# Kernel optimization log

Measured on AMD Instinct MI355X. Metric: run time of the kernel, lower is better.

Reference implementation:

```python
import jax, jax.numpy as jnp
import numpy as np

LN_EPS = 1e-5


def _segment_mean(vals, idx, num_segments):
    s = jax.ops.segment_sum(vals, idx, num_segments=num_segments)
    cnt = jax.ops.segment_sum(jnp.ones((vals.shape[0],), vals.dtype), idx, num_segments=num_segments)
    return s / jnp.maximum(cnt, 1.0)[:, None]


def _sage_layer(x, src, dst, W_l, b_l, W_r, gamma, beta):
    # PyG SAGEConv (mean aggr): out = lin_l(mean_{j in N(i)} x_j) + lin_r(x_i)
    N = x.shape[0]
    agg = _segment_mean(x[src], dst, N)                     # [N, in]
    h = agg @ W_l.T + b_l + x @ W_r.T                       # [N, out]
    mu = jnp.mean(h, axis=-1, keepdims=True)
    var = jnp.mean((h - mu) ** 2, axis=-1, keepdims=True)
    h = (h - mu) * jax.lax.rsqrt(var + LN_EPS) * gamma + beta
    return jax.nn.relu(h)                                   # dropout: eval mode (identity)


def setup_inputs() -> dict:
    key = jax.random.key(0)
    ks = jax.random.split(key, 20)
    N, E, IN, H, OUT, G, C = 50000, 600000, 128, 128, 64, 64, 2

    def glorot(k, fo, fi):
        lim = np.sqrt(6.0 / (fo + fi)).astype(np.float32)
        return jax.random.uniform(k, (fo, fi), jnp.float32, -lim, lim)

    inp = {
        'x': jax.random.normal(ks[0], (N, IN), jnp.float32),
        'edge_index': jax.random.randint(ks[1], (2, E), 0, N, jnp.int64),
        'batch': jnp.sort(jax.random.randint(ks[2], (N,), 0, G, jnp.int64)),
    }
    dims = [(IN, H), (H, H), (H, OUT)]
    for i, (fi, fo) in enumerate(dims):
        inp[f'Wl{i}'] = glorot(ks[3 + 4 * i], fo, fi)
        inp[f'bl{i}'] = jnp.zeros((fo,), jnp.float32)
        inp[f'Wr{i}'] = glorot(ks[4 + 4 * i], fo, fi)
        inp[f'g{i}'] = jnp.ones((fo,), jnp.float32)
        inp[f'be{i}'] = jnp.zeros((fo,), jnp.float32)
    inp['cW1'] = glorot(ks[16], H, 2 * OUT)
    inp['cb1'] = jnp.zeros((H,), jnp.float32)
    inp['cW2'] = glorot(ks[17], C, H)
    inp['cb2'] = jnp.zeros((C,), jnp.float32)
    return inp


def reference(x, edge_index, batch,
              Wl0, bl0, Wr0, g0, be0,
              Wl1, bl1, Wr1, g1, be1,
              Wl2, bl2, Wr2, g2, be2,
              cW1, cb1, cW2, cb2):
    src, dst = edge_index[0], edge_index[1]
    h = _sage_layer(x, src, dst, Wl0, bl0, Wr0, g0, be0)
    h = _sage_layer(h, src, dst, Wl1, bl1, Wr1, g1, be1)
    h = _sage_layer(h, src, dst, Wl2, bl2, Wr2, g2, be2)
    G = 64  # number of graphs
    x_mean = _segment_mean(h, batch, G)                     # [G, out]
    x_max = jax.ops.segment_max(h, batch, num_segments=G)   # [G, out]
    z = jnp.concatenate([x_mean, x_max], axis=-1)           # [G, 2*out]
    z = jax.nn.relu(z @ cW1.T + cb1)
    return z @ cW2.T + cb2                                  # [G, num_classes]
```

## Files before the change

kernel.cpp:

```cpp
#include <hip/hip_runtime.h>

typedef unsigned short ushort_t;
typedef short s16x8 __attribute__((ext_vector_type(8)));
typedef float f32x4 __attribute__((ext_vector_type(4)));

#define LN_EPS 1e-5f

__device__ __forceinline__ float b2f(ushort_t u) {
    return __uint_as_float(((unsigned)u) << 16);
}
__device__ __forceinline__ ushort_t f2b(float f) {
    unsigned b = __float_as_uint(f);
    b += 0x7FFFu + ((b >> 16) & 1u);
    return (ushort_t)(b >> 16);
}
__device__ __forceinline__ float ldf(const void* p, size_t i, int isF) {
    return isF ? ((const float*)p)[i] : b2f(((const ushort_t*)p)[i]);
}

__global__ void GraphSAGE_36026185678961_kernel() {}

__global__ void k_detect(const void* w0, const void* ei, int* __restrict__ flags) {
    int t = threadIdx.x;
    const ushort_t* u = (const ushort_t*)w0;
    int pass = 0;
    #pragma unroll
    for (int k = 0; k < 4; ++k) {
        ushort_t v = u[t * 4 + k];
        int ex = (v >> 7) & 0xFF;
        if (ex == 0 || (ex >= 0x60 && ex <= 0x7E)) pass++;
    }
    const unsigned* w = (const unsigned*)ei;
    int nz = (w[2 * t + 1] != 0u) ? 1 : 0;
    #pragma unroll
    for (int off = 32; off; off >>= 1) {
        pass += __shfl_down(pass, off, 64);
        nz += __shfl_down(nz, off, 64);
    }
    if (t == 0) {
        flags[0] = (pass < 205) ? 1 : 0;
        flags[1] = (nz == 0) ? 1 : 0;
    }
}

__global__ void k_zero(int* __restrict__ deg, float* __restrict__ Z, int N) {
    int i = blockIdx.x * blockDim.x + threadIdx.x;
    if (i < N) deg[i] = 0;
    if (i < 64 * 128) Z[i] = 0.f;
}

__global__ void k_xconv(const void* X, const int* __restrict__ flags,
                        ushort_t* __restrict__ XB, int total4) {
    int idx = blockIdx.x * blockDim.x + threadIdx.x;
    if (idx >= total4) return;
    if (flags[0]) {
        float4 v = ((const float4*)X)[idx];
        ushort4 o;
        o.x = f2b(v.x); o.y = f2b(v.y); o.z = f2b(v.z); o.w = f2b(v.w);
        ((ushort4*)XB)[idx] = o;
    } else {
        ((ushort4*)XB)[idx] = ((const ushort4*)X)[idx];
    }
}

__global__ void k_edges(const void* ei, int E, int N, const int* __restrict__ flags,
                        int* __restrict__ s32, int* __restrict__ d32, int* __restrict__ deg) {
    int e = blockIdx.x * blockDim.x + threadIdx.x;
    if (e >= E) return;
    int s, d;
    if (flags[1]) {
        const long long* p = (const long long*)ei;
        s = (int)p[e];
        d = (int)p[E + e];
    } else {
        const int* p = (const int*)ei;
        s = p[e];
        d = p[E + e];
    }
    s32[e] = s;
    d32[e] = d;
    if ((unsigned)d < (unsigned)N) atomicAdd(&deg[d], 1);
}

__global__ void k_scan1(const int* __restrict__ deg, int N,
                        int* __restrict__ rowptr, int* __restrict__ bsum) {
    __shared__ int wsum[4];
    __shared__ int wpre[4];
    int tid = threadIdx.x;
    int lane = tid & 63;
    int w = tid >> 6;
    int i = blockIdx.x * 256 + tid;
    int v = (i < N) ? deg[i] : 0;
    int x = v;
    #pragma unroll
    for (int off = 1; off < 64; off <<= 1) {
        int t = __shfl_up(x, off, 64);
        if (lane >= off) x += t;
    }
    if (lane == 63) wsum[w] = x;
    __syncthreads();
    if (tid == 0) {
        int a = wsum[0]; wpre[0] = a;
        a += wsum[1]; wpre[1] = a;
        a += wsum[2]; wpre[2] = a;
        a += wsum[3]; wpre[3] = a;
    }
    __syncthreads();
    int woff = (w == 0) ? 0 : wpre[w - 1];
    if (i < N) rowptr[i] = woff + x - v;
    if (tid == 0) bsum[blockIdx.x] = wpre[3];
}

__global__ void k_scan2(const int* __restrict__ bsum, int nb,
                        int* __restrict__ boff, int* __restrict__ rowptrN) {
    __shared__ int wsum[4];
    __shared__ int wpre[4];
    int tid = threadIdx.x;
    int lane = tid & 63;
    int w = tid >> 6;
    int run = 0;
    for (int base = 0; base < nb; base += 256) {
        int i = base + tid;
        int v = (i < nb) ? bsum[i] : 0;
        int x = v;
        #pragma unroll
        for (int off = 1; off < 64; off <<= 1) {
            int t = __shfl_up(x, off, 64);
            if (lane >= off) x += t;
        }
        if (lane == 63) wsum[w] = x;
        __syncthreads();
        if (tid == 0) {
            int a = wsum[0]; wpre[0] = a;
            a += wsum[1]; wpre[1] = a;
            a += wsum[2]; wpre[2] = a;
            a += wsum[3]; wpre[3] = a;
        }
        __syncthreads();
        int woff = (w == 0) ? 0 : wpre[w - 1];
        if (i < nb) boff[i] = run + woff + x - v;
        int tot = wpre[3];
        __syncthreads();
        run += tot;
    }
    if (tid == 0) *rowptrN = run;
}

__global__ void k_scan3(int* __restrict__ rowptr, const int* __restrict__ boff,
                        int* __restrict__ cursor, int N) {
    int i = blockIdx.x * 256 + threadIdx.x;
    if (i < N) {
        int r = rowptr[i] + boff[i >> 8];
        rowptr[i] = r;
        cursor[i] = r;
    }
}

__global__ void k_fill(const int* __restrict__ src, const int* __restrict__ dst, int E, int N,
                       int* __restrict__ cursor, int* __restrict__ col) {
    int e = blockIdx.x * blockDim.x + threadIdx.x;
    if (e < E) {
        int d = dst[e];
        if ((unsigned)d < (unsigned)N) {
            int p = atomicAdd(&cursor[d], 1);
            if ((unsigned)p < (unsigned)E) {
                int s = src[e];
                col[p] = ((unsigned)s < (unsigned)N) ? s : 0;
            }
        }
    }
}

__global__ void k_bounds(const void* batch, int N, int G, const int* __restrict__ flags,
                         int* __restrict__ bounds) {
    int g = threadIdx.x;
    if (g > G) return;
    int isL = flags[1];
    int lo = 0, hi = N;
    while (lo < hi) {
        int mid = (lo + hi) >> 1;
        int bv = isL ? (int)((const long long*)batch)[mid] : ((const int*)batch)[mid];
        if (bv < g) lo = mid + 1; else hi = mid;
    }
    bounds[g] = lo;
}

__global__ __launch_bounds__(256) void k_agg(
    const ushort_t* __restrict__ X, const int* __restrict__ rowptr,
    const int* __restrict__ col, ushort_t* __restrict__ AGG, int N) {
    int i = blockIdx.x * 4 + (threadIdx.x >> 6);
    if (i >= N) return;
    int l = threadIdx.x & 63;
    int half = l >> 5;
    int fq = l & 31;
    const ushort4* X4 = (const ushort4*)X;
    int s = rowptr[i], e = rowptr[i + 1];
    float a0 = 0.f, a1 = 0.f, a2 = 0.f, a3 = 0.f;
    int p = s + half;
    for (; p + 2 < e; p += 4) {
        int j0 = col[p], j1 = col[p + 2];
        ushort4 u0 = X4[(size_t)j0 * 32 + fq];
        ushort4 u1 = X4[(size_t)j1 * 32 + fq];
        a0 += b2f(u0.x) + b2f(u1.x);
        a1 += b2f(u0.y) + b2f(u1.y);
        a2 += b2f(u0.z) + b2f(u1.z);
        a3 += b2f(u0.w) + b2f(u1.w);
    }
    for (; p < e; p += 2) {
        int j = col[p];
        ushort4 u = X4[(size_t)j * 32 + fq];
        a0 += b2f(u.x); a1 += b2f(u.y); a2 += b2f(u.z); a3 += b2f(u.w);
    }
    a0 += __shfl_xor(a0, 32, 64);
    a1 += __shfl_xor(a1, 32, 64);
    a2 += __shfl_xor(a2, 32, 64);
    a3 += __shfl_xor(a3, 32, 64);
    if (half == 0) {
        int d = e - s;
        float inv = 1.f / (float)(d > 0 ? d : 1);
        ushort4 o;
        o.x = f2b(a0 * inv);
        o.y = f2b(a1 * inv);
        o.z = f2b(a2 * inv);
        o.w = f2b(a3 * inv);
        ((ushort4*)AGG)[(size_t)i * 32 + fq] = o;
    }
}

template <int FO>
__global__ void k_wprep(const void* Wl, const void* Wr, const int* __restrict__ flags,
                        ushort_t* __restrict__ Wb) {
    int t = blockIdx.x * blockDim.x + threadIdx.x;
    if (t >= 256 * FO) return;
    int isF = flags[0];
    int f = t >> 8, k = t & 255;
    float v = (k < 128) ? ldf(Wl, f * 128 + k, isF) : ldf(Wr, f * 128 + (k - 128), isF);
    Wb[t] = isF ? f2b(v) : ((const ushort_t*)((k < 128) ? Wl : Wr))[f * 128 + (k & 127)];
}

template <int FO>
__global__ __launch_bounds__(256, 1) void k_gemm_ln(
    const ushort_t* __restrict__ AGG, const ushort_t* __restrict__ X,
    const ushort_t* __restrict__ Wb,
    const void* bl, const void* gam, const void* bet,
    const int* __restrict__ flags,
    ushort_t* __restrict__ H, int M) {
    constexpr int NT = FO / 16;
    constexpr int R = 4;
    int lane = threadIdx.x & 63;
    int wid = threadIdx.x >> 6;
    int wrow0 = (blockIdx.x * 4 + wid) * (R * 16);
    if (wrow0 >= M) return;
    int isF = flags[0];
    int m = lane & 15;
    int q = lane >> 4;

    int arow[R];
    #pragma unroll
    for (int r = 0; r < R; ++r) {
        int ar = wrow0 + r * 16 + m;
        arow[r] = (ar < M) ? ar : (M - 1);
    }

    f32x4 acc[R][NT];
    #pragma unroll
    for (int r = 0; r < R; ++r)
        #pragma unroll
        for (int nt = 0; nt < NT; ++nt) acc[r][nt] = (f32x4){0.f, 0.f, 0.f, 0.f};

    #pragma unroll
    for (int kk = 0; kk < 8; ++kk) {
        const ushort_t* base = (kk < 4) ? AGG : X;
        int ko = (kk & 3) * 32 + q * 8;
        s16x8 a[R];
        #pragma unroll
        for (int r = 0; r < R; ++r)
            a[r] = *(const s16x8*)(base + (size_t)arow[r] * 128 + ko);
        #pragma unroll
        for (int nt = 0; nt < NT; ++nt) {
            s16x8 b = *(const s16x8*)(Wb + (size_t)(nt * 16 + m) * 256 + kk * 32 + q * 8);
            #pragma unroll
            for (int r = 0; r < R; ++r)
                acc[r][nt] = __builtin_amdgcn_mfma_f32_16x16x32_bf16(a[r], b, acc[r][nt], 0, 0, 0);
        }
    }

    #pragma unroll
    for (int r = 0; r < R; ++r) {
        #pragma unroll
        for (int nt = 0; nt < NT; ++nt) {
            float bv = ldf(bl, nt * 16 + m, isF);
            #pragma unroll
            for (int rr = 0; rr < 4; ++rr) acc[r][nt][rr] += bv;
        }
        float mu[4], rs[4];
        #pragma unroll
        for (int rr = 0; rr < 4; ++rr) {
            float s1 = 0.f, s2 = 0.f;
            #pragma unroll
            for (int nt = 0; nt < NT; ++nt) {
                float v = acc[r][nt][rr];
                s1 += v;
                s2 += v * v;
            }
            #pragma unroll
            for (int off = 1; off < 16; off <<= 1) {
                s1 += __shfl_xor(s1, off, 64);
                s2 += __shfl_xor(s2, off, 64);
            }
            float mm = s1 / (float)FO;
            float var = s2 / (float)FO - mm * mm;
            var = var > 0.f ? var : 0.f;
            mu[rr] = mm;
            rs[rr] = rsqrtf(var + LN_EPS);
        }
        #pragma unroll
        for (int nt = 0; nt < NT; ++nt) {
            int n0 = nt * 16 + m;
            float g = ldf(gam, n0, isF);
            float be = ldf(bet, n0, isF);
            #pragma unroll
            for (int rr = 0; rr < 4; ++rr) {
                int row = wrow0 + r * 16 + q * 4 + rr;
                if (row < M) {
                    float y = (acc[r][nt][rr] - mu[rr]) * rs[rr] * g + be;
                    y = y > 0.f ? y : 0.f;
                    H[(size_t)row * FO + n0] = f2b(y);
                }
            }
        }
    }
}

__global__ void k_pool(const ushort_t* __restrict__ H,
                       const int* __restrict__ bounds, float* __restrict__ Z, int N) {
    int g = blockIdx.x >> 3;
    int chunk = blockIdx.x & 7;
    int f = threadIdx.x & 63;
    int sub = threadIdx.x >> 6;
    int strm = chunk * 4 + sub;
    int s = bounds[g], e = bounds[g + 1];
    s = s < 0 ? 0 : (s > N ? N : s);
    e = e < s ? s : (e > N ? N : e);
    float sum = 0.f, mx = 0.f;
    for (int i = s + strm; i < e; i += 32) {
        float v = b2f(H[(size_t)i * 64 + f]);
        sum += v;
        mx = mx > v ? mx : v;
    }
    atomicAdd(&Z[g * 128 + f], sum);
    atomicMax((int*)&Z[g * 128 + 64 + f], __float_as_int(mx));
}

__global__ void k_mlp(const float* __restrict__ Z, const int* __restrict__ bounds,
                      const void* cW1, const void* cb1, const void* cW2, const void* cb2,
                      const int* __restrict__ flags, void* __restrict__ out) {
    int g = blockIdx.x;
    int f = threadIdx.x;
    int isF = flags[0];
    __shared__ float z[128];
    __shared__ float hid[128];
    __shared__ float r0[2], r1[2];
    int cnt = bounds[g + 1] - bounds[g];
    float c = (float)(cnt > 0 ? cnt : 1);
    float zv = Z[g * 128 + f];
    if (f < 64) zv /= c;
    z[f] = zv;
    __syncthreads();
    float acc = ldf(cb1, f, isF);
    #pragma unroll 8
    for (int k = 0; k < 128; ++k) acc += z[k] * ldf(cW1, f * 128 + k, isF);
    acc = acc > 0.f ? acc : 0.f;
    hid[f] = acc;
    __syncthreads();
    float p0 = hid[f] * ldf(cW2, f, isF);
    float p1 = hid[f] * ldf(cW2, 128 + f, isF);
    #pragma unroll
    for (int off = 32; off > 0; off >>= 1) {
        p0 += __shfl_xor(p0, off, 64);
        p1 += __shfl_xor(p1, off, 64);
    }
    int w = f >> 6;
    if ((f & 63) == 0) { r0[w] = p0; r1[w] = p1; }
    __syncthreads();
    if (f == 0) {
        float v0 = r0[0] + r0[1] + ldf(cb2, 0, isF);
        float v1 = r1[0] + r1[1] + ldf(cb2, 1, isF);
        if (isF) {
            ((float*)out)[g * 2 + 0] = v0;
            ((float*)out)[g * 2 + 1] = v1;
        } else {
            ((ushort_t*)out)[g * 2 + 0] = f2b(v0);
            ((ushort_t*)out)[g * 2 + 1] = f2b(v1);
        }
    }
}

extern "C" void kernel_launch(void* const* d_in, const int* in_sizes, int n_in,
                              void* d_out, int out_size, void* d_ws, size_t ws_size,
                              hipStream_t stream) {
    const void* x = d_in[0];
    const void* ei = d_in[1];
    const void* batch = d_in[2];
    const void* Wl0 = d_in[3];
    const void* bl0 = d_in[4];
    const void* Wr0 = d_in[5];
    const void* g0 = d_in[6];
    const void* be0 = d_in[7];
    const void* Wl1 = d_in[8];
    const void* bl1 = d_in[9];
    const void* Wr1 = d_in[10];
    const void* g1 = d_in[11];
    const void* be1 = d_in[12];
    const void* Wl2 = d_in[13];
    const void* bl2 = d_in[14];
    const void* Wr2 = d_in[15];
    const void* g2 = d_in[16];
    const void* be2 = d_in[17];
    const void* cW1 = d_in[18];
    const void* cb1 = d_in[19];
    const void* cW2 = d_in[20];
    const void* cb2 = d_in[21];

    const int N = in_sizes[0] / 128;
    const int E = in_sizes[1] / 2;
    const int G = 64;

    char* w = (char*)d_ws;
    size_t o = 0;
    auto take = [&](size_t bytes) -> void* {
        void* p = w + o;
        o = (o + bytes + 255) & ~(size_t)255;
        return p;
    };
    int nb1 = (N + 255) / 256;
    int* flags  = (int*)take(4 * 4);
    int* rowptr = (int*)take((size_t)(N + 1) * 4);
    int* cursor = (int*)take((size_t)N * 4);
    int* deg    = (int*)take((size_t)N * 4);
    int* bsum   = (int*)take((size_t)nb1 * 4);
    int* boff   = (int*)take((size_t)nb1 * 4);
    int* col    = (int*)take((size_t)E * 4);
    int* src32  = (int*)take((size_t)E * 4);
    int* dst32  = (int*)take((size_t)E * 4);
    int* bounds = (int*)take((size_t)(G + 1) * 4);
    float* Z    = (float*)take((size_t)G * 128 * 4);
    ushort_t* Wb0 = (ushort_t*)take((size_t)128 * 256 * 2);
    ushort_t* Wb1 = (ushort_t*)take((size_t)128 * 256 * 2);
    ushort_t* Wb2 = (ushort_t*)take((size_t)64 * 256 * 2);
    ushort_t* AGG = (ushort_t*)take((size_t)N * 128 * 2);
    ushort_t* H1  = (ushort_t*)take((size_t)N * 128 * 2);
    ushort_t* H2  = (ushort_t*)take((size_t)N * 128 * 2);
    ushort_t* XB  = H2;
    ushort_t* H3  = H1;
    if (o > ws_size) return;

    int eb = (E + 255) / 256;
    k_detect<<<1, 64, 0, stream>>>(Wl0, ei, flags);
    k_zero<<<nb1, 256, 0, stream>>>(deg, Z, N);
    k_xconv<<<(N * 128 / 4 + 255) / 256, 256, 0, stream>>>(x, flags, XB, N * 128 / 4);
    k_edges<<<eb, 256, 0, stream>>>(ei, E, N, flags, src32, dst32, deg);
    k_scan1<<<nb1, 256, 0, stream>>>(deg, N, rowptr, bsum);
    k_scan2<<<1, 256, 0, stream>>>(bsum, nb1, boff, rowptr + N);
    k_scan3<<<nb1, 256, 0, stream>>>(rowptr, boff, cursor, N);
    k_fill<<<eb, 256, 0, stream>>>(src32, dst32, E, N, cursor, col);
    k_bounds<<<1, 128, 0, stream>>>(batch, N, G, flags, bounds);
    k_wprep<128><<<128, 256, 0, stream>>>(Wl0, Wr0, flags, Wb0);
    k_wprep<128><<<128, 256, 0, stream>>>(Wl1, Wr1, flags, Wb1);
    k_wprep<64><<<64, 256, 0, stream>>>(Wl2, Wr2, flags, Wb2);

    int gb = (N + 255) / 256;
    int ab = (N + 3) / 4;

    k_agg<<<ab, 256, 0, stream>>>(XB, rowptr, col, AGG, N);
    k_gemm_ln<128><<<gb, 256, 0, stream>>>(AGG, XB, Wb0, bl0, g0, be0, flags, H1, N);
    k_agg<<<ab, 256, 0, stream>>>(H1, rowptr, col, AGG, N);
    k_gemm_ln<128><<<gb, 256, 0, stream>>>(AGG, H1, Wb1, bl1, g1, be1, flags, H2, N);
    k_agg<<<ab, 256, 0, stream>>>(H2, rowptr, col, AGG, N);
    k_gemm_ln<64><<<gb, 256, 0, stream>>>(AGG, H2, Wb2, bl2, g2, be2, flags, H3, N);

    k_pool<<<G * 8, 256, 0, stream>>>(H3, bounds, Z, N);
    k_mlp<<<G, 128, 0, stream>>>(Z, bounds, cW1, cb1, cW2, cb2, flags, d_out);
}
```

Measured before the change: 393.1 us.

## Merge small setup kernels, widen aggregation loads, and raise GEMM occupancy

Folds the detect and zero kernels into one launch, moves the batch bounds search into scan2, and merges the three weight-prep launches into one, cutting the launch count. The aggregation kernel now loads 16-byte rows (8 bf16) per lane with four edge groups per wave instead of two, then reduces across lane quarters with shuffles. The LN GEMM launch bounds allow two blocks per CU, which may increase register pressure or spilling.

```diff
diff --git a/kernel.cpp b/kernel.cpp
--- a/kernel.cpp
+++ b/kernel.cpp
@@ -14,39 +14,42 @@
     b += 0x7FFFu + ((b >> 16) & 1u);
     return (ushort_t)(b >> 16);
 }
+__device__ __forceinline__ unsigned f2b2(float lo, float hi) {
+    return (unsigned)f2b(lo) | ((unsigned)f2b(hi) << 16);
+}
 __device__ __forceinline__ float ldf(const void* p, size_t i, int isF) {
     return isF ? ((const float*)p)[i] : b2f(((const ushort_t*)p)[i]);
 }
 
 __global__ void GraphSAGE_36026185678961_kernel() {}
 
-__global__ void k_detect(const void* w0, const void* ei, int* __restrict__ flags) {
-    int t = threadIdx.x;
-    const ushort_t* u = (const ushort_t*)w0;
-    int pass = 0;
-    #pragma unroll
-    for (int k = 0; k < 4; ++k) {
-        ushort_t v = u[t * 4 + k];
-        int ex = (v >> 7) & 0xFF;
-        if (ex == 0 || (ex >= 0x60 && ex <= 0x7E)) pass++;
-    }
-    const unsigned* w = (const unsigned*)ei;
-    int nz = (w[2 * t + 1] != 0u) ? 1 : 0;
-    #pragma unroll
-    for (int off = 32; off; off >>= 1) {
-        pass += __shfl_down(pass, off, 64);
-        nz += __shfl_down(nz, off, 64);
-    }
-    if (t == 0) {
-        flags[0] = (pass < 205) ? 1 : 0;
-        flags[1] = (nz == 0) ? 1 : 0;
-    }
-}
-
-__global__ void k_zero(int* __restrict__ deg, float* __restrict__ Z, int N) {
+__global__ void k_detect_zero(const void* w0, const void* ei, int* __restrict__ flags,
+                              int* __restrict__ deg, float* __restrict__ Z, int N) {
     int i = blockIdx.x * blockDim.x + threadIdx.x;
     if (i < N) deg[i] = 0;
     if (i < 64 * 128) Z[i] = 0.f;
+    if (blockIdx.x == 0 && threadIdx.x < 64) {
+        int t = threadIdx.x;
+        const ushort_t* u = (const ushort_t*)w0;
+        int pass = 0;
+        #pragma unroll
+        for (int k = 0; k < 4; ++k) {
+            ushort_t v = u[t * 4 + k];
+            int ex = (v >> 7) & 0xFF;
+            if (ex == 0 || (ex >= 0x60 && ex <= 0x7E)) pass++;
+        }
+        const unsigned* w = (const unsigned*)ei;
+        int nz = (w[2 * t + 1] != 0u) ? 1 : 0;
+        #pragma unroll
+        for (int off = 32; off; off >>= 1) {
+            pass += __shfl_down(pass, off, 64);
+            nz += __shfl_down(nz, off, 64);
+        }
+        if (t == 0) {
+            flags[0] = (pass < 205) ? 1 : 0;
+            flags[1] = (nz == 0) ? 1 : 0;
+        }
+    }
 }
 
 __global__ void k_xconv(const void* X, const int* __restrict__ flags,
@@ -112,7 +115,9 @@
 }
 
 __global__ void k_scan2(const int* __restrict__ bsum, int nb,
-                        int* __restrict__ boff, int* __restrict__ rowptrN) {
+                        int* __restrict__ boff, int* __restrict__ rowptrN,
+                        const void* batch, int N, int G, const int* __restrict__ flags,
+                        int* __restrict__ bounds) {
     __shared__ int wsum[4];
     __shared__ int wpre[4];
     int tid = threadIdx.x;
@@ -144,6 +149,16 @@
         run += tot;
     }
     if (tid == 0) *rowptrN = run;
+    if (tid <= G) {
+        int isL = flags[1];
+        int lo = 0, hi = N;
+        while (lo < hi) {
+            int mid = (lo + hi) >> 1;
+            int bv = isL ? (int)((const long long*)batch)[mid] : ((const int*)batch)[mid];
+            if (bv < tid) lo = mid + 1; else hi = mid;
+        }
+        bounds[tid] = lo;
+    }
 }
 
 __global__ void k_scan3(int* __restrict__ rowptr, const int* __restrict__ boff,
@@ -171,75 +186,81 @@
     }
 }
 
-__global__ void k_bounds(const void* batch, int N, int G, const int* __restrict__ flags,
-                         int* __restrict__ bounds) {
-    int g = threadIdx.x;
-    if (g > G) return;
-    int isL = flags[1];
-    int lo = 0, hi = N;
-    while (lo < hi) {
-        int mid = (lo + hi) >> 1;
-        int bv = isL ? (int)((const long long*)batch)[mid] : ((const int*)batch)[mid];
-        if (bv < g) lo = mid + 1; else hi = mid;
-    }
-    bounds[g] = lo;
-}
-
 __global__ __launch_bounds__(256) void k_agg(
     const ushort_t* __restrict__ X, const int* __restrict__ rowptr,
     const int* __restrict__ col, ushort_t* __restrict__ AGG, int N) {
     int i = blockIdx.x * 4 + (threadIdx.x >> 6);
     if (i >= N) return;
     int l = threadIdx.x & 63;
-    int half = l >> 5;
-    int fq = l & 31;
-    const ushort4* X4 = (const ushort4*)X;
+    int qn = l >> 4;
+    int fo = l & 15;
+    const uint4* X8 = (const uint4*)X;
     int s = rowptr[i], e = rowptr[i + 1];
-    float a0 = 0.f, a1 = 0.f, a2 = 0.f, a3 = 0.f;
-    int p = s + half;
-    for (; p + 2 < e; p += 4) {
-        int j0 = col[p], j1 = col[p + 2];
-        ushort4 u0 = X4[(size_t)j0 * 32 + fq];
-        ushort4 u1 = X4[(size_t)j1 * 32 + fq];
-        a0 += b2f(u0.x) + b2f(u1.x);
-        a1 += b2f(u0.y) + b2f(u1.y);
-        a2 += b2f(u0.z) + b2f(u1.z);
-        a3 += b2f(u0.w) + b2f(u1.w);
-    }
-    for (; p < e; p += 2) {
+    float al[4] = {0.f, 0.f, 0.f, 0.f};
+    float ah[4] = {0.f, 0.f, 0.f, 0.f};
+    int p = s + qn;
+    for (; p + 4 < e; p += 8) {
+        int j0 = col[p], j1 = col[p + 4];
+        uint4 u0 = X8[(size_t)j0 * 16 + fo];
+        uint4 u1 = X8[(size_t)j1 * 16 + fo];
+        unsigned w0[4] = {u0.x, u0.y, u0.z, u0.w};
+        unsigned w1[4] = {u1.x, u1.y, u1.z, u1.w};
+        #pragma unroll
+        for (int k = 0; k < 4; ++k) {
+            al[k] += __uint_as_float(w0[k] << 16) + __uint_as_float(w1[k] << 16);
+            ah[k] += __uint_as_float(w0[k] & 0xFFFF0000u) + __uint_as_float(w1[k] & 0xFFFF0000u);
+        }
+    }
+    for (; p < e; p += 4) {
         int j = col[p];
-        ushort4 u = X4[(size_t)j * 32 + fq];
-        a0 += b2f(u.x); a1 += b2f(u.y); a2 += b2f(u.z); a3 += b2f(u.w);
-    }
-    a0 += __shfl_xor(a0, 32, 64);
-    a1 += __shfl_xor(a1, 32, 64);
-    a2 += __shfl_xor(a2, 32, 64);
-    a3 += __shfl_xor(a3, 32, 64);
-    if (half == 0) {
+        uint4 u = X8[(size_t)j * 16 + fo];
+        unsigned w0[4] = {u.x, u.y, u.z, u.w};
+        #pragma unroll
+        for (int k = 0; k < 4; ++k) {
+            al[k] += __uint_as_float(w0[k] << 16);
+            ah[k] += __uint_as_float(w0[k] & 0xFFFF0000u);
+        }
+    }
+    #pragma unroll
+    for (int k = 0; k < 4; ++k) {
+        al[k] += __shfl_xor(al[k], 16, 64);
+        al[k] += __shfl_xor(al[k], 32, 64);
+        ah[k] += __shfl_xor(ah[k], 16, 64);
+        ah[k] += __shfl_xor(ah[k], 32, 64);
+    }
+    if (qn == 0) {
         int d = e - s;
         float inv = 1.f / (float)(d > 0 ? d : 1);
-        ushort4 o;
-        o.x = f2b(a0 * inv);
-        o.y = f2b(a1 * inv);
-        o.z = f2b(a2 * inv);
-        o.w = f2b(a3 * inv);
-        ((ushort4*)AGG)[(size_t)i * 32 + fq] = o;
-    }
+        uint4 o;
+        o.x = f2b2(al[0] * inv, ah[0] * inv);
+        o.y = f2b2(al[1] * inv, ah[1] * inv);
+        o.z = f2b2(al[2] * inv, ah[2] * inv);
+        o.w = f2b2(al[3] * inv, ah[3] * inv);
+        ((uint4*)AGG)[(size_t)i * 16 + fo] = o;
+    }
+}
+
+__global__ void k_wprep(const void* Wl0, const void* Wr0, const void* Wl1, const void* Wr1,
+                        const void* Wl2, const void* Wr2, const int* __restrict__ flags,
+                        ushort_t* __restrict__ Wb0, ushort_t* __restrict__ Wb1,
+                        ushort_t* __restrict__ Wb2) {
+    int t = blockIdx.x * blockDim.x + threadIdx.x;
+    int isF = flags[0];
+    const void* Wl;
+    const void* Wr;
+    ushort_t* Wb;
+    int base;
+    if (t < 256 * 128) { Wl = Wl0; Wr = Wr0; Wb = Wb0; base = t; }
+    else if (t < 2 * 256 * 128) { Wl = Wl1; Wr = Wr1; Wb = Wb1; base = t - 256 * 128; }
+    else if (t < 2 * 256 * 128 + 256 * 64) { Wl = Wl2; Wr = Wr2; Wb = Wb2; base = t - 2 * 256 * 128; }
+    else return;
+    int f = base >> 8, k = base & 255;
+    float v = (k < 128) ? ldf(Wl, f * 128 + k, isF) : ldf(Wr, f * 128 + (k - 128), isF);
+    Wb[base] = isF ? f2b(v) : ((const ushort_t*)((k < 128) ? Wl : Wr))[f * 128 + (k & 127)];
 }
 
 template <int FO>
-__global__ void k_wprep(const void* Wl, const void* Wr, const int* __restrict__ flags,
-                        ushort_t* __restrict__ Wb) {
-    int t = blockIdx.x * blockDim.x + threadIdx.x;
-    if (t >= 256 * FO) return;
-    int isF = flags[0];
-    int f = t >> 8, k = t & 255;
-    float v = (k < 128) ? ldf(Wl, f * 128 + k, isF) : ldf(Wr, f * 128 + (k - 128), isF);
-    Wb[t] = isF ? f2b(v) : ((const ushort_t*)((k < 128) ? Wl : Wr))[f * 128 + (k & 127)];
-}
-
-template <int FO>
-__global__ __launch_bounds__(256, 1) void k_gemm_ln(
+__global__ __launch_bounds__(256, 2) void k_gemm_ln(
     const ushort_t* __restrict__ AGG, const ushort_t* __restrict__ X,
     const ushort_t* __restrict__ Wb,
     const void* bl, const void* gam, const void* bet,
@@ -456,18 +477,15 @@
     if (o > ws_size) return;
 
     int eb = (E + 255) / 256;
-    k_detect<<<1, 64, 0, stream>>>(Wl0, ei, flags);
-    k_zero<<<nb1, 256, 0, stream>>>(deg, Z, N);
+    k_detect_zero<<<nb1, 256, 0, stream>>>(Wl0, ei, flags, deg, Z, N);
     k_xconv<<<(N * 128 / 4 + 255) / 256, 256, 0, stream>>>(x, flags, XB, N * 128 / 4);
     k_edges<<<eb, 256, 0, stream>>>(ei, E, N, flags, src32, dst32, deg);
     k_scan1<<<nb1, 256, 0, stream>>>(deg, N, rowptr, bsum);
-    k_scan2<<<1, 256, 0, stream>>>(bsum, nb1, boff, rowptr + N);
+    k_scan2<<<1, 256, 0, stream>>>(bsum, nb1, boff, rowptr + N, batch, N, G, flags, bounds);
     k_scan3<<<nb1, 256, 0, stream>>>(rowptr, boff, cursor, N);
     k_fill<<<eb, 256, 0, stream>>>(src32, dst32, E, N, cursor, col);
-    k_bounds<<<1, 128, 0, stream>>>(batch, N, G, flags, bounds);
-    k_wprep<128><<<128, 256, 0, stream>>>(Wl0, Wr0, flags, Wb0);
-    k_wprep<128><<<128, 256, 0, stream>>>(Wl1, Wr1, flags, Wb1);
-    k_wprep<64><<<64, 256, 0, stream>>>(Wl2, Wr2, flags, Wb2);
+    k_wprep<<<(2 * 256 * 128 + 256 * 64 + 255) / 256, 256, 0, stream>>>(
+        Wl0, Wr0, Wl1, Wr1, Wl2, Wr2, flags, Wb0, Wb1, Wb2);
 
     int gb = (N + 255) / 256;
     int ab = (N + 3) / 4;
```

After: 379.9 us. 1.03x faster.
